# Kernel optimization log

Measured on AMD Instinct MI355X. Metric: run time of the kernel, lower is better.

The kernel has to match this reference:

```python
import jax, jax.numpy as jnp
import numpy as np

N = 100000
E = 1600000
NUM_GRAPHS = 128
IN_C = 11
HID = 128


def setup_inputs() -> dict:
    key = jax.random.key(0)
    ks = jax.random.split(key, 16)
    x = jax.random.normal(ks[0], (N, IN_C), dtype=jnp.float32)
    edge_index = jax.random.randint(ks[1], (2, E), 0, N, dtype=jnp.int64)
    batch = jnp.sort(jax.random.randint(ks[2], (N,), 0, NUM_GRAPHS, dtype=jnp.int64))
    s_in = 1.0 / np.sqrt(IN_C)
    s_h = 1.0 / np.sqrt(HID)
    params = {
        'W1': jax.random.normal(ks[3], (IN_C, HID), jnp.float32) * s_in,
        'b1': jnp.zeros((HID,), jnp.float32),
        'W2': jax.random.normal(ks[4], (HID, HID), jnp.float32) * s_h,
        'b2': jnp.zeros((HID,), jnp.float32),
        'W4': jax.random.normal(ks[5], (HID, HID), jnp.float32) * s_h,
        'b4': jnp.zeros((HID,), jnp.float32),
        'Wd1': jax.random.normal(ks[6], (HID, HID), jnp.float32) * s_h,
        'bd1': jnp.zeros((HID,), jnp.float32),
        'Wd2': jax.random.normal(ks[7], (HID, HID), jnp.float32) * s_h,
        'bd2': jnp.zeros((HID,), jnp.float32),
        'Wo': jax.random.normal(ks[8], (HID, 1), jnp.float32) * s_h,
        'bo': jnp.zeros((1,), jnp.float32),
    }
    return {'x': x, 'edge_index': edge_index, 'batch': batch, **params}


def _gcn_norm(edge_index, n_nodes):
    # add self loops, compute symmetric normalization (PyG GCNConv defaults)
    loop = jnp.arange(n_nodes, dtype=edge_index.dtype)
    row = jnp.concatenate([edge_index[0], loop])
    col = jnp.concatenate([edge_index[1], loop])
    deg = jax.ops.segment_sum(jnp.ones_like(col, dtype=jnp.float32), col,
                              num_segments=n_nodes)
    dinv = jnp.where(deg > 0, jax.lax.rsqrt(deg), 0.0)
    norm = dinv[row] * dinv[col]  # [E+N]
    return row, col, norm


def _gcn_conv(h, row, col, norm, W, b, n_nodes):
    h = h @ W  # dense lin first (PyG order)
    msg = norm[:, None] * h[row]            # gather + normalize
    out = jax.ops.segment_sum(msg, col, num_segments=n_nodes)  # scatter-add
    return out + b


def reference(x, edge_index, batch, W1, b1, W2, b2, W4, b4,
              Wd1, bd1, Wd2, bd2, Wo, bo):
    n = x.shape[0]
    row, col, norm = _gcn_norm(edge_index, n)
    # dropout is identity in eval mode
    h = jax.nn.relu(_gcn_conv(x, row, col, norm, W1, b1, n))
    h = jax.nn.relu(_gcn_conv(h, row, col, norm, W2, b2, n))
    h = _gcn_conv(h, row, col, norm, W4, b4, n)
    # global_mean_pool over batch ids
    sums = jax.ops.segment_sum(h, batch, num_segments=NUM_GRAPHS)
    cnts = jax.ops.segment_sum(jnp.ones((n,), jnp.float32), batch,
                               num_segments=NUM_GRAPHS)
    g = sums / jnp.maximum(cnts, 1.0)[:, None]  # [NUM_GRAPHS, HID]
    g = jax.nn.relu(g @ Wd1 + bd1)
    g = jax.nn.relu(g @ Wd2 + bd2)
    return g @ Wo + bo  # [NUM_GRAPHS, 1]
```

## Files before the change

kernel.cpp:

```cpp
#include <hip/hip_runtime.h>
#include <hip/hip_fp16.h>

#define HIDDEN 128
#define BSHIFT 8
#define BMASK 255
#define CHUNK 6144
#define BCAP 6144

typedef _Float16 h8 __attribute__((ext_vector_type(8)));
typedef float f4x __attribute__((ext_vector_type(4)));

__global__ __launch_bounds__(256) void fill_bin(const int* __restrict__ row,
                                                const int* __restrict__ col,
                                                int* __restrict__ bcnt,
                                                int2* __restrict__ ptmp, int E) {
    __shared__ int cnt[512], start[512], place[512], gbase[512];
    __shared__ int ssum[256];
    __shared__ int2 stage[CHUNK];
    int t = threadIdx.x;
    int e0 = blockIdx.x * CHUNK;
    int e1 = min(e0 + CHUNK, E);
    cnt[t] = 0; cnt[t + 256] = 0;
    __syncthreads();
    for (int e = e0 + t; e < e1; e += 256)
        atomicAdd(&cnt[col[e] >> BSHIFT], 1);
    __syncthreads();
    int s2 = cnt[2 * t] + cnt[2 * t + 1];
    ssum[t] = s2;
    __syncthreads();
    for (int d = 1; d < 256; d <<= 1) {
        int v = (t >= d) ? ssum[t - d] : 0;
        __syncthreads();
        ssum[t] += v;
        __syncthreads();
    }
    int excl = ssum[t] - s2;
    start[2 * t] = excl;
    start[2 * t + 1] = excl + cnt[2 * t];
    place[2 * t] = excl;
    place[2 * t + 1] = excl + cnt[2 * t];
    __syncthreads();
    for (int e = e0 + t; e < e1; e += 256) {
        int c = col[e], r = row[e];
        int slot = atomicAdd(&place[c >> BSHIFT], 1);
        stage[slot] = make_int2(r, c);
    }
    {
        int c0 = cnt[t], c1 = cnt[t + 256];
        if (c0 > 0) gbase[t] = atomicAdd(&bcnt[t], c0);
        if (c1 > 0) gbase[t + 256] = atomicAdd(&bcnt[t + 256], c1);
    }
    __syncthreads();
    int n = e1 - e0;
    for (int i = t; i < n; i += 256) {
        int2 p = stage[i];
        int b = p.y >> BSHIFT;
        ptmp[(size_t)b * BCAP + gbase[b] + (i - start[b])] = p;
    }
}

__global__ __launch_bounds__(512) void scan_buckets(const int* __restrict__ bcnt,
                                                    int* __restrict__ bbase, int NB) {
    __shared__ int s[512];
    int t = threadIdx.x;
    int v0 = (t < NB) ? bcnt[t] : 0;
    s[t] = v0;
    __syncthreads();
    for (int d = 1; d < 512; d <<= 1) {
        int v = (t >= d) ? s[t - d] : 0;
        __syncthreads();
        s[t] += v;
        __syncthreads();
    }
    bbase[t] = s[t] - v0;
}

__global__ __launch_bounds__(256) void fill_scatter(const int2* __restrict__ ptmp,
                                                    const int* __restrict__ bcnt,
                                                    const int* __restrict__ bbase,
                                                    int* __restrict__ offsets,
                                                    float* __restrict__ dinv,
                                                    int* __restrict__ sorted_r,
                                                    int N, int E) {
    __shared__ int2 stage[BCAP];
    __shared__ int cnt[256], loff[256], cur[256];
    int b = blockIdx.x, t = threadIdx.x;
    int m = bcnt[b];
    int base = bbase[b];
    int nbase = b << BSHIFT;
    cnt[t] = 0;
    __syncthreads();
    for (int i = t; i < m; i += 256) {
        int2 p = ptmp[(size_t)b * BCAP + i];
        stage[i] = p;
        atomicAdd(&cnt[p.y & BMASK], 1);
    }
    __syncthreads();
    int my = cnt[t];
    loff[t] = my;
    __syncthreads();
    for (int d = 1; d < 256; d <<= 1) {
        int v = (t >= d) ? loff[t - d] : 0;
        __syncthreads();
        loff[t] += v;
        __syncthreads();
    }
    int excl = loff[t] - my;
    cur[t] = excl;
    int node = nbase + t;
    if (node < N) {
        offsets[node] = base + excl;
        dinv[node] = rsqrtf((float)(my + 1));
    }
    if (b == gridDim.x - 1 && t == 0) offsets[N] = E;
    __syncthreads();
    for (int i = t; i < m; i += 256) {
        int2 p = stage[i];
        int slot = atomicAdd(&cur[p.y & BMASK], 1);
        sorted_r[base + slot] = p.x;
    }
}

__global__ __launch_bounds__(256) void pad_x(const float* __restrict__ x,
                                             const float* __restrict__ dinv,
                                             __half* __restrict__ xp, int N) {
    int q = blockIdx.x * 256 + threadIdx.x;
    if (q >= N * 16) return;
    int i = q >> 4, c = q & 15;
    float v = (c < 11) ? x[(size_t)i * 11 + c] * dinv[i] : 0.f;
    xp[q] = __float2half(v);
}

__global__ __launch_bounds__(256) void agg16(const __half* __restrict__ xp,
                                             float* __restrict__ aggx,
                                             const int* __restrict__ offsets,
                                             const int* __restrict__ sorted_r,
                                             const float* __restrict__ dinv, int N) {
    int wid  = (blockIdx.x * 256 + threadIdx.x) >> 6;
    int lane = threadIdx.x & 63;
    if (wid >= N) return;
    int c = wid;
    int g = lane >> 3, cp = lane & 7;
    int beg = offsets[c], end = offsets[c + 1];
    const __half2* xp2 = (const __half2*)xp;
    float ax = 0.f, ay = 0.f;
    if (g == 0) {
        float2 v = __half22float2(xp2[(size_t)c * 8 + cp]);
        ax = v.x; ay = v.y;
    }
    for (int idx = beg + g; idx < end; idx += 8) {
        int r = sorted_r[idx];
        float2 v = __half22float2(xp2[(size_t)r * 8 + cp]);
        ax += v.x; ay += v.y;
    }
    ax += __shfl_xor(ax, 32); ay += __shfl_xor(ay, 32);
    ax += __shfl_xor(ax, 16); ay += __shfl_xor(ay, 16);
    ax += __shfl_xor(ax, 8);  ay += __shfl_xor(ay, 8);
    if (lane < 8) {
        float dc = dinv[c];
        aggx[(size_t)c * 16 + cp * 2]     = ax * dc;
        aggx[(size_t)c * 16 + cp * 2 + 1] = ay * dc;
    }
}

__global__ __launch_bounds__(256) void gemm_in_agg(const float* __restrict__ aggx,
                                                   const float* __restrict__ W1,
                                                   __half* __restrict__ out, int N) {
    int i = blockIdx.x * 2 + (threadIdx.x >> 7);
    int j = threadIdx.x & 127;
    if (i >= N) return;
    float acc = 0.f;
#pragma unroll
    for (int c = 0; c < 11; ++c) acc += aggx[(size_t)i * 16 + c] * W1[c * HIDDEN + j];
    out[(size_t)i * HIDDEN + j] = __float2half(acc);
}

__global__ __launch_bounds__(256) void pack_w(const float* __restrict__ W,
                                              const float* __restrict__ bias,
                                              __half* __restrict__ packed) {
    int q = blockIdx.x * 256 + threadIdx.x;
    if (q < 2048) {
        int s = q >> 9, rem = q & 511, ct = rem >> 6, l = rem & 63;
        int b = l >> 4, n = l & 15;
        __half hi8[8], lo8[8];
#pragma unroll
        for (int i = 0; i < 8; ++i) {
            float w = W[(s * 32 + b * 8 + i) * HIDDEN + ct * 16 + n];
            __half h = __float2half(w);
            hi8[i] = h;
            lo8[i] = __float2half(w - __half2float(h));
        }
        *(uint4*)(packed + (size_t)q * 8)         = *(uint4*)hi8;
        *(uint4*)(packed + 16384 + (size_t)q * 8) = *(uint4*)lo8;
    }
    if (q < 128) packed[32768 + q] = __float2half(bias[q]);
}

__global__ __launch_bounds__(256) void gemm_mfma(const __half* __restrict__ H,
                                                 const __half* __restrict__ packed,
                                                 const float* __restrict__ dinv,
                                                 __half* __restrict__ out, int N) {
    __shared__ __half Wl[32768];
    for (int q = threadIdx.x; q < 4096; q += 256)
        ((uint4*)Wl)[q] = ((const uint4*)packed)[q];
    int l = threadIdx.x & 63, wv = threadIdx.x >> 6;
    int m = l & 15, b = l >> 4;
    const __half* bias_h = packed + 32768;
    __syncthreads();

    f4x acc[2][8];
#pragma unroll
    for (int t = 0; t < 2; ++t)
#pragma unroll
        for (int ct = 0; ct < 8; ++ct) acc[t][ct] = (f4x){0.f, 0.f, 0.f, 0.f};

    int rowA0 = blockIdx.x * 128 + wv * 32 + m;

#pragma unroll
    for (int s = 0; s < 4; ++s) {
        uint4 bv = *(const uint4*)(bias_h + s * 32 + b * 8);
        __half2* bh = (__half2*)&bv;
        h8 a[2];
#pragma unroll
        for (int t = 0; t < 2; ++t) {
            int row = rowA0 + t * 16;
            uint4 av = make_uint4(0u, 0u, 0u, 0u);
            if (row < N) av = *(const uint4*)(H + (size_t)row * HIDDEN + s * 32 + b * 8);
            __half2* ah = (__half2*)&av;
#pragma unroll
            for (int p = 0; p < 4; ++p) {
                float2 f  = __half22float2(ah[p]);
                float2 bf = __half22float2(bh[p]);
                ah[p] = __floats2half2_rn(fmaxf(f.x + bf.x, 0.f), fmaxf(f.y + bf.y, 0.f));
            }
            a[t] = *(h8*)&av;
        }
#pragma unroll
        for (int ct = 0; ct < 8; ++ct) {
            h8 whi = *(h8*)&Wl[((s * 8 + ct) * 64 + l) * 8];
            h8 wlo = *(h8*)&Wl[16384 + ((s * 8 + ct) * 64 + l) * 8];
#pragma unroll
            for (int t = 0; t < 2; ++t) {
                acc[t][ct] = __builtin_amdgcn_mfma_f32_16x16x32_f16(a[t], whi, acc[t][ct], 0, 0, 0);
                acc[t][ct] = __builtin_amdgcn_mfma_f32_16x16x32_f16(a[t], wlo, acc[t][ct], 0, 0, 0);
            }
        }
    }
#pragma unroll
    for (int t = 0; t < 2; ++t) {
        int rbase = blockIdx.x * 128 + wv * 32 + t * 16 + b * 4;
#pragma unroll
        for (int i = 0; i < 4; ++i) {
            int row = rbase + i;
            if (row < N) {
                float dv = dinv[row];
#pragma unroll
                for (int ct = 0; ct < 8; ++ct)
                    out[(size_t)row * HIDDEN + ct * 16 + m] = __float2half(acc[t][ct][i] * dv);
            }
        }
    }
}

__global__ __launch_bounds__(256) void agg128h(const __half* __restrict__ src,
                                               __half* __restrict__ dst,
                                               const int* __restrict__ offsets,
                                               const int* __restrict__ sorted_r,
                                               const float* __restrict__ dinv, int N) {
    int wid  = (blockIdx.x * 256 + threadIdx.x) >> 6;
    int lane = threadIdx.x & 63;
    if (wid >= N) return;
    int c = wid;
    int beg = offsets[c], end = offsets[c + 1];
    int g = lane >> 4, sub = lane & 15;
    const uint4* hp = (const uint4*)src;
    float a0=0.f,a1=0.f,a2=0.f,a3=0.f,a4=0.f,a5=0.f,a6=0.f,a7=0.f;

    auto accum = [&](uint4 u) {
        __half2 p0 = *(__half2*)&u.x, p1 = *(__half2*)&u.y;
        __half2 p2 = *(__half2*)&u.z, p3 = *(__half2*)&u.w;
        float2 f0 = __half22float2(p0), f1 = __half22float2(p1);
        float2 f2 = __half22float2(p2), f3 = __half22float2(p3);
        a0 += f0.x; a1 += f0.y; a2 += f1.x; a3 += f1.y;
        a4 += f2.x; a5 += f2.y; a6 += f3.x; a7 += f3.y;
    };

    if (g == 0) accum(hp[(size_t)c * 16 + sub]);

    int i = beg;
    for (; i + 16 <= end; i += 16) {
        int base = i + 4 * g;
        int r0 = sorted_r[base + 0];
        int r1 = sorted_r[base + 1];
        int r2 = sorted_r[base + 2];
        int r3 = sorted_r[base + 3];
        uint4 u0 = hp[(size_t)r0 * 16 + sub];
        uint4 u1 = hp[(size_t)r1 * 16 + sub];
        uint4 u2 = hp[(size_t)r2 * 16 + sub];
        uint4 u3 = hp[(size_t)r3 * 16 + sub];
        accum(u0); accum(u1); accum(u2); accum(u3);
    }
    for (int idx = i + g; idx < end; idx += 4) {
        accum(hp[(size_t)sorted_r[idx] * 16 + sub]);
    }
    a0 += __shfl_xor(a0, 32); a1 += __shfl_xor(a1, 32);
    a2 += __shfl_xor(a2, 32); a3 += __shfl_xor(a3, 32);
    a4 += __shfl_xor(a4, 32); a5 += __shfl_xor(a5, 32);
    a6 += __shfl_xor(a6, 32); a7 += __shfl_xor(a7, 32);
    a0 += __shfl_xor(a0, 16); a1 += __shfl_xor(a1, 16);
    a2 += __shfl_xor(a2, 16); a3 += __shfl_xor(a3, 16);
    a4 += __shfl_xor(a4, 16); a5 += __shfl_xor(a5, 16);
    a6 += __shfl_xor(a6, 16); a7 += __shfl_xor(a7, 16);
    if (g == 0) {
        float dc = dinv[c];
        __half2 h01 = __floats2half2_rn(a0 * dc, a1 * dc);
        __half2 h23 = __floats2half2_rn(a2 * dc, a3 * dc);
        __half2 h45 = __floats2half2_rn(a4 * dc, a5 * dc);
        __half2 h67 = __floats2half2_rn(a6 * dc, a7 * dc);
        uint4 o;
        o.x = *(unsigned int*)&h01; o.y = *(unsigned int*)&h23;
        o.z = *(unsigned int*)&h45; o.w = *(unsigned int*)&h67;
        ((uint4*)dst)[(size_t)c * 16 + sub] = o;
    }
}

__global__ __launch_bounds__(256) void pool_partial(const __half* __restrict__ h,
                                                    const int* __restrict__ batch,
                                                    float* __restrict__ partials, int N) {
    int g = blockIdx.x >> 3, part8 = blockIdx.x & 7;
    int t = threadIdx.x, cp = t & 63, rp = t >> 6;
    int lo = 0, hi = N;
    while (lo < hi) { int m = (lo + hi) >> 1; if (batch[m] < g) lo = m + 1; else hi = m; }
    int beg = lo;
    lo = beg; hi = N;
    while (lo < hi) { int m = (lo + hi) >> 1; if (batch[m] < g + 1) lo = m + 1; else hi = m; }
    int end = lo;
    const __half2* h2 = (const __half2*)h;
    float ax = 0.f, ay = 0.f;
    for (int i = beg + part8 * 4 + rp; i < end; i += 32) {
        float2 v = __half22float2(h2[(size_t)i * 64 + cp]);
        ax += v.x; ay += v.y;
    }
    __shared__ float px[4][64], py[4][64];
    px[rp][cp] = ax; py[rp][cp] = ay;
    __syncthreads();
    if (rp == 0) {
        float sx = px[0][cp] + px[1][cp] + px[2][cp] + px[3][cp];
        float sy = py[0][cp] + py[1][cp] + py[2][cp] + py[3][cp];
        partials[(size_t)blockIdx.x * 128 + cp * 2]     = sx;
        partials[(size_t)blockIdx.x * 128 + cp * 2 + 1] = sy;
    }
}

__global__ __launch_bounds__(128) void head_kernel(const float* __restrict__ partials,
                                                   const int* __restrict__ batch,
                                                   const float* __restrict__ b4,
                                                   const float* __restrict__ Wd1,
                                                   const float* __restrict__ bd1,
                                                   const float* __restrict__ Wd2,
                                                   const float* __restrict__ bd2,
                                                   const float* __restrict__ Wo,
                                                   const float* __restrict__ bo,
                                                   float* __restrict__ out, int N) {
    int g = blockIdx.x;
    int j = threadIdx.x;
    __shared__ float sA[128], sB[128], red[128];
    int lo = 0, hi = N;
    while (lo < hi) { int m = (lo + hi) >> 1; if (batch[m] < g) lo = m + 1; else hi = m; }
    int beg = lo;
    lo = beg; hi = N;
    while (lo < hi) { int m = (lo + hi) >> 1; if (batch[m] < g + 1) lo = m + 1; else hi = m; }
    int cnt = lo - beg;
    float s = 0.f;
#pragma unroll
    for (int p = 0; p < 8; ++p) s += partials[(size_t)(g * 8 + p) * 128 + j];
    sA[j] = (cnt > 0) ? s / (float)cnt + b4[j] : 0.f;
    __syncthreads();
    float a = bd1[j];
#pragma unroll 4
    for (int k = 0; k < 128; ++k) a += sA[k] * Wd1[k * HIDDEN + j];
    sB[j] = fmaxf(a, 0.f);
    __syncthreads();
    a = bd2[j];
#pragma unroll 4
    for (int k = 0; k < 128; ++k) a += sB[k] * Wd2[k * HIDDEN + j];
    red[j] = fmaxf(a, 0.f) * Wo[j];
    __syncthreads();
    for (int d = 64; d > 0; d >>= 1) {
        if (j < d) red[j] += red[j + d];
        __syncthreads();
    }
    if (j == 0) out[g] = red[0] + bo[0];
}

extern "C" void kernel_launch(void* const* d_in, const int* in_sizes, int n_in,
                              void* d_out, int out_size, void* d_ws, size_t ws_size,
                              hipStream_t stream) {
    const float* x   = (const float*)d_in[0];
    const int*   ei  = (const int*)d_in[1];
    const int*   bat = (const int*)d_in[2];
    const float* W1  = (const float*)d_in[3];
    const float* b1  = (const float*)d_in[4];
    const float* W2  = (const float*)d_in[5];
    const float* b2  = (const float*)d_in[6];
    const float* W4  = (const float*)d_in[7];
    const float* b4  = (const float*)d_in[8];
    const float* Wd1 = (const float*)d_in[9];
    const float* bd1 = (const float*)d_in[10];
    const float* Wd2 = (const float*)d_in[11];
    const float* bd2 = (const float*)d_in[12];
    const float* Wo  = (const float*)d_in[13];
    const float* bo  = (const float*)d_in[14];
    float* out = (float*)d_out;

    const int N = in_sizes[0] / 11;
    const int E = in_sizes[1] / 2;
    const int* row = ei;
    const int* col = ei + E;
    const int B = (N + (1 << BSHIFT) - 1) >> BSHIFT;

    size_t off = 0;
    auto carve = [&](size_t bytes) {
        void* p = (char*)d_ws + off;
        off += (bytes + 255) & ~(size_t)255;
        return p;
    };
    __half* bufHA    = (__half*)carve((size_t)N * HIDDEN * 2);
    __half* bufHB    = (__half*)carve((size_t)N * HIDDEN * 2);
    __half* xp       = (__half*)carve((size_t)N * 16 * 2);
    float*  aggx     = (float*)carve((size_t)N * 16 * 4);
    int*    offsets  = (int*)carve((size_t)(N + 1) * 4);
    float*  dinv     = (float*)carve((size_t)N * 4);
    int*    sorted_r = (int*)carve((size_t)E * 4);
    int*    bcnt     = (int*)carve((size_t)512 * 4);
    int*    bbase    = (int*)carve((size_t)512 * 4);
    float*  partials = (float*)carve((size_t)128 * 8 * 128 * 4);
    __half* packW2   = (__half*)carve((size_t)(32768 + 128) * 2);
    __half* packW4   = (__half*)carve((size_t)(32768 + 128) * 2);
    int2* ptmp = (int2*)bufHA;
    (void)ws_size; (void)n_in; (void)out_size;

    hipMemsetAsync(bcnt, 0, (size_t)512 * 4, stream);
    fill_bin<<<(E + CHUNK - 1) / CHUNK, 256, 0, stream>>>(row, col, bcnt, ptmp, E);
    scan_buckets<<<1, 512, 0, stream>>>(bcnt, bbase, B);
    fill_scatter<<<B, 256, 0, stream>>>(ptmp, bcnt, bbase, offsets, dinv,
                                        sorted_r, N, E);

    pack_w<<<8, 256, 0, stream>>>(W2, b1, packW2);
    pack_w<<<8, 256, 0, stream>>>(W4, b2, packW4);

    int aggBlocks  = (N + 3) / 4;
    int mfmaBlocks = (N + 127) / 128;

    pad_x<<<(N * 16 + 255) / 256, 256, 0, stream>>>(x, dinv, xp, N);
    agg16<<<aggBlocks, 256, 0, stream>>>(xp, aggx, offsets, sorted_r, dinv, N);
    gemm_in_agg<<<(N + 1) / 2, 256, 0, stream>>>(aggx, W1, bufHA, N);
    gemm_mfma<<<mfmaBlocks, 256, 0, stream>>>(bufHA, packW2, dinv, bufHB, N);
    agg128h<<<aggBlocks, 256, 0, stream>>>(bufHB, bufHA, offsets, sorted_r, dinv, N);
    gemm_mfma<<<mfmaBlocks, 256, 0, stream>>>(bufHA, packW4, dinv, bufHB, N);
    agg128h<<<aggBlocks, 256, 0, stream>>>(bufHB, bufHA, offsets, sorted_r, dinv, N);
    pool_partial<<<128 * 8, 256, 0, stream>>>(bufHA, bat, partials, N);
    head_kernel<<<128, 128, 0, stream>>>(partials, bat, b4, Wd1, bd1, Wd2, bd2,
                                         Wo, bo, out, N);
}
```

Measured before the change: 340.8 us.

## Hold GEMM weights in registers with persistent grid and transposed MFMA

```diff
diff --git a/kernel.cpp b/kernel.cpp
--- a/kernel.cpp
+++ b/kernel.cpp
@@ -4,7 +4,7 @@
 #define HIDDEN 128
 #define BSHIFT 8
 #define BMASK 255
-#define CHUNK 6144
+#define CHUNK 4096
 #define BCAP 6144
 
 typedef _Float16 h8 __attribute__((ext_vector_type(8)));
@@ -196,67 +196,64 @@
     if (q < 128) packed[32768 + q] = __float2half(bias[q]);
 }
 
-__global__ __launch_bounds__(256) void gemm_mfma(const __half* __restrict__ H,
-                                                 const __half* __restrict__ packed,
-                                                 const float* __restrict__ dinv,
-                                                 __half* __restrict__ out, int N) {
-    __shared__ __half Wl[32768];
-    for (int q = threadIdx.x; q < 4096; q += 256)
-        ((uint4*)Wl)[q] = ((const uint4*)packed)[q];
+__global__ __launch_bounds__(256, 2) void gemm_mfma(const __half* __restrict__ H,
+                                                    const __half* __restrict__ packed,
+                                                    const float* __restrict__ dinv,
+                                                    __half* __restrict__ out,
+                                                    int N, int ngroups) {
     int l = threadIdx.x & 63, wv = threadIdx.x >> 6;
-    int m = l & 15, b = l >> 4;
+    int cthalf = wv & 1;
+    int n16 = l & 15, koct = l >> 4;
+    h8 whi[4][4], wlo[4][4];
+#pragma unroll
+    for (int s = 0; s < 4; ++s)
+#pragma unroll
+        for (int mt = 0; mt < 4; ++mt) {
+            int ct = cthalf * 4 + mt;
+            whi[s][mt] = *(const h8*)(packed + (size_t)((s * 8 + ct) * 64 + l) * 8);
+            wlo[s][mt] = *(const h8*)(packed + 16384 + (size_t)((s * 8 + ct) * 64 + l) * 8);
+        }
+    h8 biasf[4];
     const __half* bias_h = packed + 32768;
-    __syncthreads();
-
-    f4x acc[2][8];
-#pragma unroll
-    for (int t = 0; t < 2; ++t)
-#pragma unroll
-        for (int ct = 0; ct < 8; ++ct) acc[t][ct] = (f4x){0.f, 0.f, 0.f, 0.f};
-
-    int rowA0 = blockIdx.x * 128 + wv * 32 + m;
-
-#pragma unroll
-    for (int s = 0; s < 4; ++s) {
-        uint4 bv = *(const uint4*)(bias_h + s * 32 + b * 8);
-        __half2* bh = (__half2*)&bv;
-        h8 a[2];
-#pragma unroll
-        for (int t = 0; t < 2; ++t) {
-            int row = rowA0 + t * 16;
-            uint4 av = make_uint4(0u, 0u, 0u, 0u);
-            if (row < N) av = *(const uint4*)(H + (size_t)row * HIDDEN + s * 32 + b * 8);
-            __half2* ah = (__half2*)&av;
+#pragma unroll
+    for (int s = 0; s < 4; ++s)
+        biasf[s] = *(const h8*)(bias_h + s * 32 + koct * 8);
+
+    for (int g = blockIdx.x * 2 + (wv >> 1); g < ngroups; g += gridDim.x * 2) {
+        int node = g * 16 + n16;
+        bool ok = node < N;
+        f4x acc[4];
+#pragma unroll
+        for (int mt = 0; mt < 4; ++mt) acc[mt] = (f4x){0.f, 0.f, 0.f, 0.f};
+#pragma unroll
+        for (int s = 0; s < 4; ++s) {
+            uint4 bv = make_uint4(0u, 0u, 0u, 0u);
+            if (ok) bv = *(const uint4*)(H + (size_t)node * HIDDEN + s * 32 + koct * 8);
+            __half2* bh2 = (__half2*)&bv;
+            const __half2* bb = (const __half2*)&biasf[s];
 #pragma unroll
             for (int p = 0; p < 4; ++p) {
-                float2 f  = __half22float2(ah[p]);
-                float2 bf = __half22float2(bh[p]);
-                ah[p] = __floats2half2_rn(fmaxf(f.x + bf.x, 0.f), fmaxf(f.y + bf.y, 0.f));
+                float2 f  = __half22float2(bh2[p]);
+                float2 bf = __half22float2(bb[p]);
+                bh2[p] = __floats2half2_rn(fmaxf(f.x + bf.x, 0.f), fmaxf(f.y + bf.y, 0.f));
             }
-            a[t] = *(h8*)&av;
-        }
-#pragma unroll
-        for (int ct = 0; ct < 8; ++ct) {
-            h8 whi = *(h8*)&Wl[((s * 8 + ct) * 64 + l) * 8];
-            h8 wlo = *(h8*)&Wl[16384 + ((s * 8 + ct) * 64 + l) * 8];
-#pragma unroll
-            for (int t = 0; t < 2; ++t) {
-                acc[t][ct] = __builtin_amdgcn_mfma_f32_16x16x32_f16(a[t], whi, acc[t][ct], 0, 0, 0);
-                acc[t][ct] = __builtin_amdgcn_mfma_f32_16x16x32_f16(a[t], wlo, acc[t][ct], 0, 0, 0);
+            h8 bfrag = *(h8*)&bv;
+#pragma unroll
+            for (int mt = 0; mt < 4; ++mt) {
+                acc[mt] = __builtin_amdgcn_mfma_f32_16x16x32_f16(whi[s][mt], bfrag, acc[mt], 0, 0, 0);
+                acc[mt] = __builtin_amdgcn_mfma_f32_16x16x32_f16(wlo[s][mt], bfrag, acc[mt], 0, 0, 0);
             }
         }
-    }
-#pragma unroll
-    for (int t = 0; t < 2; ++t) {
-        int rbase = blockIdx.x * 128 + wv * 32 + t * 16 + b * 4;
-#pragma unroll
-        for (int i = 0; i < 4; ++i) {
-            int row = rbase + i;
-            if (row < N) {
-                float dv = dinv[row];
-#pragma unroll
-                for (int ct = 0; ct < 8; ++ct)
-                    out[(size_t)row * HIDDEN + ct * 16 + m] = __float2half(acc[t][ct][i] * dv);
+        if (ok) {
+            float dv = dinv[node];
+#pragma unroll
+            for (int mt = 0; mt < 4; ++mt) {
+                int ch = (cthalf * 4 + mt) * 16 + koct * 4;
+                __half2 h01 = __floats2half2_rn(acc[mt][0] * dv, acc[mt][1] * dv);
+                __half2 h23 = __floats2half2_rn(acc[mt][2] * dv, acc[mt][3] * dv);
+                uint2 o;
+                o.x = *(unsigned int*)&h01; o.y = *(unsigned int*)&h23;
+                *(uint2*)(out + (size_t)node * HIDDEN + ch) = o;
             }
         }
     }
@@ -418,6 +415,7 @@
     const int* row = ei;
     const int* col = ei + E;
     const int B = (N + (1 << BSHIFT) - 1) >> BSHIFT;
+    const int ngroups = (N + 15) / 16;
 
     size_t off = 0;
     auto carve = [&](size_t bytes) {
@@ -449,15 +447,14 @@
     pack_w<<<8, 256, 0, stream>>>(W2, b1, packW2);
     pack_w<<<8, 256, 0, stream>>>(W4, b2, packW4);
 
-    int aggBlocks  = (N + 3) / 4;
-    int mfmaBlocks = (N + 127) / 128;
+    int aggBlocks = (N + 3) / 4;
 
     pad_x<<<(N * 16 + 255) / 256, 256, 0, stream>>>(x, dinv, xp, N);
     agg16<<<aggBlocks, 256, 0, stream>>>(xp, aggx, offsets, sorted_r, dinv, N);
     gemm_in_agg<<<(N + 1) / 2, 256, 0, stream>>>(aggx, W1, bufHA, N);
-    gemm_mfma<<<mfmaBlocks, 256, 0, stream>>>(bufHA, packW2, dinv, bufHB, N);
+    gemm_mfma<<<1024, 256, 0, stream>>>(bufHA, packW2, dinv, bufHB, N, ngroups);
     agg128h<<<aggBlocks, 256, 0, stream>>>(bufHB, bufHA, offsets, sorted_r, dinv, N);
-    gemm_mfma<<<mfmaBlocks, 256, 0, stream>>>(bufHA, packW4, dinv, bufHB, N);
+    gemm_mfma<<<1024, 256, 0, stream>>>(bufHA, packW4, dinv, bufHB, N, ngroups);
     agg128h<<<aggBlocks, 256, 0, stream>>>(bufHB, bufHA, offsets, sorted_r, dinv, N);
     pool_partial<<<128 * 8, 256, 0, stream>>>(bufHA, bat, partials, N);
     head_kernel<<<128, 128, 0, stream>>>(partials, bat, b4, Wd1, bd1, Wd2, bd2,
```

Result: faster. 333.6 us (-2.1%).
